# Optimization experiments

Measured on AMD Instinct MI355X. Metric: run time of the kernel, lower is better.

## Reference

```python
import jax, jax.numpy as jnp
import numpy as np

N_NODES = 50000
N_EDGES = 625000
F_IN = 128
F_OUT = 128


def setup_inputs() -> dict:
    key = jax.random.key(0)
    k_x, k_w, k_v, k_r, k_c = jax.random.split(key, 5)
    # Xavier-uniform bound for weight init (matches nn.init.xavier_uniform_)
    bound = float(np.sqrt(6.0 / (F_IN + F_OUT)))
    return {
        "x": jax.random.normal(k_x, (N_NODES, F_IN), dtype=jnp.float32),
        "weight": jax.random.uniform(k_w, (F_IN, F_OUT), minval=-bound, maxval=bound, dtype=jnp.float32),
        "bias": jnp.zeros((F_OUT,), dtype=jnp.float32),
        "edge_vals": jax.random.uniform(k_v, (N_EDGES,), dtype=jnp.float32),
        "edge_rows": jax.random.randint(k_r, (N_EDGES,), 0, N_NODES, dtype=jnp.int32),
        "edge_cols": jax.random.randint(k_c, (N_EDGES,), 0, N_NODES, dtype=jnp.int32),
    }


def reference(x, weight, bias, edge_vals, edge_rows, edge_cols):
    # support = input @ weight  (dense GEMM)  -> [N, F_out]
    support = x @ weight
    # output = spmm(adj, support): for each edge (r, c, v): out[r] += v * support[c]
    msgs = support[edge_cols] * edge_vals[:, None]          # [E, F_out] gather
    out = jax.ops.segment_sum(msgs, edge_rows, num_segments=N_NODES)  # scatter-add
    return out + bias
```

## Files before the change

### kernel.cpp

```cpp
#include <hip/hip_runtime.h>
#include <hip/hip_bf16.h>


#define F_DIM 128

#define NBC 98
#define SLABC 7360
#define NROW_PAD (NBC * 512)

#define BIN_T 256
#define BIN_EPT 16
#define BIN_CHUNK (BIN_T * BIN_EPT)

#define SPLIT_T 512
#define SPLIT_EPT 15

typedef short bf16x8 __attribute__((ext_vector_type(8)));
typedef float f32x4 __attribute__((ext_vector_type(4)));

__device__ __forceinline__ unsigned short f2bf(float f) {
    unsigned int u = __float_as_uint(f);
    u += 0x7FFFu + ((u >> 16) & 1u);
    return (unsigned short)(u >> 16);
}

__global__ void __launch_bounds__(BIN_T)
k1_kernel(const int* __restrict__ rows, const int* __restrict__ cols,
          const float* __restrict__ vals, int* __restrict__ lenC,
          uint2* __restrict__ ebinC, int n_edges,
          const float* __restrict__ w, unsigned short* __restrict__ wt,
          int nbin) {
    __shared__ int lcnt[NBC];
    __shared__ int lbase[NBC];
    __shared__ int garr[NBC];
    __shared__ int partial[128];
    __shared__ uint2 srec[BIN_CHUNK];
    __shared__ unsigned char sbkt[BIN_CHUNK];

    const int t = threadIdx.x;

    if ((int)blockIdx.x >= nbin) {
        int idx = (blockIdx.x - nbin) * BIN_T + t;
        int n = idx >> 7, k = idx & 127;
        wt[n * F_DIM + k] = f2bf(w[k * F_DIM + n]);
        return;
    }

    const int base = blockIdx.x * BIN_CHUNK;

    for (int i = t; i < NBC; i += BIN_T) lcnt[i] = 0;
    __syncthreads();

    unsigned int mykey[BIN_EPT];
    float myval[BIN_EPT];
    bool myok[BIN_EPT];
#pragma unroll
    for (int j = 0; j < BIN_EPT; j++) {
        int e = base + j * BIN_T + t;
        myok[j] = (e < n_edges);
        if (myok[j]) {
            int r = rows[e];
            int c = cols[e];
            myval[j] = vals[e];
            mykey[j] = ((unsigned)r << 16) | (unsigned)c;
            atomicAdd(&lcnt[r >> 9], 1);
        }
    }
    __syncthreads();

    if (t < 128) partial[t] = (t < NBC) ? lcnt[t] : 0;
    __syncthreads();
    for (int d = 1; d < 128; d <<= 1) {
        int u = (t < 128 && t >= d) ? partial[t - d] : 0;
        __syncthreads();
        if (t < 128) partial[t] += u;
        __syncthreads();
    }
    if (t < NBC) {
        lbase[t] = partial[t] - lcnt[t];
        if (lcnt[t] > 0)
            garr[t] = t * SLABC + atomicAdd(&lenC[t], lcnt[t]);
    }
    __syncthreads();
    if (t < NBC) lcnt[t] = lbase[t];
    __syncthreads();

#pragma unroll
    for (int j = 0; j < BIN_EPT; j++) {
        if (myok[j]) {
            int b = (int)(mykey[j] >> 25);
            int p = atomicAdd(&lcnt[b], 1);
            srec[p] = make_uint2(mykey[j], __float_as_uint(myval[j]));
            sbkt[p] = (unsigned char)b;
        }
    }
    __syncthreads();

    const int m = min(BIN_CHUNK, n_edges - base);
    for (int i = t; i < m; i += BIN_T) {
        int b = sbkt[i];
        int dst = garr[b] + (i - lbase[b]);
        if (dst < (b + 1) * SLABC) ebinC[dst] = srec[i];
    }
}

__global__ void __launch_bounds__(SPLIT_T)
split_kernel(const int* __restrict__ lenC, const uint2* __restrict__ ebinC,
             uint2* __restrict__ ebin2, int* __restrict__ roff,
             int* __restrict__ rlen) {
    __shared__ int cnt[SPLIT_T];
    __shared__ int lb[SPLIT_T];
    __shared__ int pos[SPLIT_T];
    __shared__ uint2 srec[SLABC];

    const int b = blockIdx.x;
    const int t = threadIdx.x;
    const int n = min(lenC[b], SLABC);
    const uint2* src = ebinC + (size_t)b * SLABC;

    cnt[t] = 0;
    __syncthreads();

    uint2 myr[SPLIT_EPT];
    int myrow[SPLIT_EPT];
#pragma unroll
    for (int j = 0; j < SPLIT_EPT; j++) {
        int idx = j * SPLIT_T + t;
        myrow[j] = -1;
        if (idx < n) {
            myr[j] = src[idx];
            myrow[j] = (int)((myr[j].x >> 16) & 511u);
            atomicAdd(&cnt[myrow[j]], 1);
        }
    }
    __syncthreads();

    int myc = cnt[t];
    pos[t] = myc;
    __syncthreads();
    for (int d = 1; d < SPLIT_T; d <<= 1) {
        int u = (t >= d) ? pos[t - d] : 0;
        __syncthreads();
        pos[t] += u;
        __syncthreads();
    }
    lb[t] = pos[t] - myc;
    __syncthreads();
    pos[t] = lb[t];
    __syncthreads();

#pragma unroll
    for (int j = 0; j < SPLIT_EPT; j++) {
        if (myrow[j] >= 0) {
            int p = atomicAdd(&pos[myrow[j]], 1);
            srec[p] = myr[j];
        }
    }
    __syncthreads();

    const int gbase = b * SLABC;
    for (int i = t; i < n; i += SPLIT_T)
        ebin2[gbase + i] = srec[i];
    roff[(b << 9) + t] = gbase + lb[t];
    rlen[(b << 9) + t] = myc;
}

__global__ void __launch_bounds__(256)
gemm_mfma_kernel(const float* __restrict__ x, const unsigned short* __restrict__ wt,
                 unsigned short* __restrict__ support) {
    const int tid = threadIdx.x;
    const int wid = tid >> 6;
    const int lane = tid & 63;
    const int l15 = lane & 15;
    const int lhi = lane >> 4;

    const int m0 = blockIdx.x * 16;
    const int n0 = wid * 32;

    const float* xrow = x + (size_t)(m0 + l15) * F_DIM + lhi * 8;
    const unsigned short* wrow0 = wt + (size_t)(n0 + l15) * F_DIM + lhi * 8;
    const unsigned short* wrow1 = wrow0 + 16 * F_DIM;

    f32x4 acc0 = {0.f, 0.f, 0.f, 0.f};
    f32x4 acc1 = {0.f, 0.f, 0.f, 0.f};
#pragma unroll
    for (int k0 = 0; k0 < F_DIM; k0 += 32) {
        float4 xa = *reinterpret_cast<const float4*>(xrow + k0);
        float4 xb = *reinterpret_cast<const float4*>(xrow + k0 + 4);
        bf16x8 a, b0, b1;
        a[0] = (short)f2bf(xa.x); a[1] = (short)f2bf(xa.y);
        a[2] = (short)f2bf(xa.z); a[3] = (short)f2bf(xa.w);
        a[4] = (short)f2bf(xb.x); a[5] = (short)f2bf(xb.y);
        a[6] = (short)f2bf(xb.z); a[7] = (short)f2bf(xb.w);
        b0 = *reinterpret_cast<const bf16x8*>(wrow0 + k0);
        b1 = *reinterpret_cast<const bf16x8*>(wrow1 + k0);
        acc0 = __builtin_amdgcn_mfma_f32_16x16x32_bf16(a, b0, acc0, 0, 0, 0);
        acc1 = __builtin_amdgcn_mfma_f32_16x16x32_bf16(a, b1, acc1, 0, 0, 0);
    }

    unsigned short* sp = support + (size_t)(m0 + 4 * lhi) * F_DIM + n0 + l15;
#pragma unroll
    for (int i = 0; i < 4; i++) {
        sp[(size_t)i * F_DIM]      = f2bf(acc0[i]);
        sp[(size_t)i * F_DIM + 16] = f2bf(acc1[i]);
    }
}

__global__ void __launch_bounds__(256)
bspmm_kernel(const unsigned short* __restrict__ support,
             const uint2* __restrict__ ebin2, const int* __restrict__ roff,
             const int* __restrict__ rlen, const float* __restrict__ bias,
             float* __restrict__ out, int n_nodes) {
    const int row = blockIdx.x * 4 + (threadIdx.x >> 6);
    const int lane = threadIdx.x & 63;
    const unsigned foff = lane * 2u;
    if (row >= n_nodes) return;

    const int s = roff[row];
    const int n = rlen[row];

    float accx = 0.f, accy = 0.f;

#define GATHER(K) (*reinterpret_cast<const unsigned*>(                        \
        support + (size_t)((K) & 0xffffu) * F_DIM + foff))
#define ACC(KEY, VAL, SV)                                                     \
    {                                                                         \
        float v = __uint_as_float(VAL);                                       \
        accx += v * __uint_as_float((SV) << 16);                              \
        accy += v * __uint_as_float((SV) & 0xFFFF0000u);                      \
    }

    int i = 0;
#pragma unroll 1
    for (; i + 3 < n; i += 4) {
        uint2 r0 = ebin2[s + i];
        uint2 r1 = ebin2[s + i + 1];
        uint2 r2 = ebin2[s + i + 2];
        uint2 r3 = ebin2[s + i + 3];
        unsigned s0 = GATHER(r0.x);
        unsigned s1 = GATHER(r1.x);
        unsigned s2 = GATHER(r2.x);
        unsigned s3 = GATHER(r3.x);
        ACC(r0.x, r0.y, s0)
        ACC(r1.x, r1.y, s1)
        ACC(r2.x, r2.y, s2)
        ACC(r3.x, r3.y, s3)
    }
#pragma unroll 1
    for (; i < n; i++) {
        uint2 r = ebin2[s + i];
        unsigned sv = GATHER(r.x);
        ACC(r.x, r.y, sv)
    }
#undef GATHER
#undef ACC

    const float2 bb = *reinterpret_cast<const float2*>(bias + foff);
    float2 o = make_float2(accx + bb.x, accy + bb.y);
    *reinterpret_cast<float2*>(out + (size_t)row * F_DIM + foff) = o;
}

extern "C" void kernel_launch(void* const* d_in, const int* in_sizes, int n_in,
                              void* d_out, int out_size, void* d_ws, size_t ws_size,
                              hipStream_t stream) {
    const float* x      = (const float*)d_in[0];
    const float* weight = (const float*)d_in[1];
    const float* bias   = (const float*)d_in[2];
    const float* evals  = (const float*)d_in[3];
    const int*   erows  = (const int*)d_in[4];
    const int*   ecols  = (const int*)d_in[5];
    float* out = (float*)d_out;

    const int n_nodes = in_sizes[0] / F_DIM;
    const int n_edges = in_sizes[3];

    unsigned short* support = (unsigned short*)d_ws;
    unsigned short* wt      = support + (size_t)n_nodes * F_DIM;
    int* lenC = (int*)(wt + F_DIM * F_DIM);
    int* roff = lenC + 128;
    int* rlen = roff + NROW_PAD;
    uintptr_t ep = (uintptr_t)(rlen + NROW_PAD);
    ep = (ep + 15) & ~(uintptr_t)15;
    uint2* ebinC = (uint2*)ep;
    uint2* ebin2 = ebinC + (size_t)NBC * SLABC;

    hipMemsetAsync(lenC, 0, NBC * sizeof(int), stream);

    int nbin = (n_edges + BIN_CHUNK - 1) / BIN_CHUNK;
    k1_kernel<<<nbin + 64, BIN_T, 0, stream>>>(erows, ecols, evals, lenC,
                                               ebinC, n_edges, weight, wt, nbin);

    split_kernel<<<NBC, SPLIT_T, 0, stream>>>(lenC, ebinC, ebin2, roff, rlen);

    gemm_mfma_kernel<<<n_nodes / 16, 256, 0, stream>>>(x, wt, support);

    bspmm_kernel<<<(n_nodes + 3) / 4, 256, 0, stream>>>(support, ebin2, roff,
                                                        rlen, bias, out, n_nodes);
}
```

Baseline: 93.98 us.

## Use wave-shuffle scans in binning kernels and half-wave edge split in SpMM

The binning and split kernels replace their shared-memory Hillis-Steele prefix scans, which need a barrier per step, with wavefront shuffle scans plus a small cross-wave combine. The binning chunk per block is halved, which launches more blocks and increases contention on the global atomics into lenC. The SpMM kernel now has each half-wave process alternate edges with 8-byte gathers covering 4 features per lane. The two halves are combined with a shuffle-xor at the end, doubling the edges in flight per row at the cost of an extra reduction and idle lanes on the final store.

Result: faster. 90.03 us (-4.2%).

```diff
diff --git a/kernel.cpp b/kernel.cpp
--- a/kernel.cpp
+++ b/kernel.cpp
@@ -9,7 +9,7 @@
 #define NROW_PAD (NBC * 512)
 
 #define BIN_T 256
-#define BIN_EPT 16
+#define BIN_EPT 8
 #define BIN_CHUNK (BIN_T * BIN_EPT)
 
 #define SPLIT_T 512
@@ -33,7 +33,7 @@
     __shared__ int lcnt[NBC];
     __shared__ int lbase[NBC];
     __shared__ int garr[NBC];
-    __shared__ int partial[128];
+    __shared__ int w0sum;
     __shared__ uint2 srec[BIN_CHUNK];
     __shared__ unsigned char sbkt[BIN_CHUNK];
 
@@ -48,7 +48,7 @@
 
     const int base = blockIdx.x * BIN_CHUNK;
 
-    for (int i = t; i < NBC; i += BIN_T) lcnt[i] = 0;
+    if (t < NBC) lcnt[t] = 0;
     __syncthreads();
 
     unsigned int mykey[BIN_EPT];
@@ -68,21 +68,26 @@
     }
     __syncthreads();
 
-    if (t < 128) partial[t] = (t < NBC) ? lcnt[t] : 0;
-    __syncthreads();
-    for (int d = 1; d < 128; d <<= 1) {
-        int u = (t < 128 && t >= d) ? partial[t - d] : 0;
-        __syncthreads();
-        if (t < 128) partial[t] += u;
-        __syncthreads();
-    }
+    const int lane = t & 63;
+    int cval = 0, inc = 0;
+    if (t < 128) {
+        cval = (t < NBC) ? lcnt[t] : 0;
+        inc = cval;
+#pragma unroll
+        for (int d = 1; d < 64; d <<= 1) {
+            int u = __shfl_up(inc, d);
+            if (lane >= d) inc += u;
+        }
+        if (t == 63) w0sum = inc;
+    }
+    __syncthreads();
+    if (t >= 64 && t < 128) inc += w0sum;
     if (t < NBC) {
-        lbase[t] = partial[t] - lcnt[t];
-        if (lcnt[t] > 0)
-            garr[t] = t * SLABC + atomicAdd(&lenC[t], lcnt[t]);
-    }
-    __syncthreads();
-    if (t < NBC) lcnt[t] = lbase[t];
+        int lb = inc - cval;
+        lbase[t] = lb;
+        if (cval > 0) garr[t] = t * SLABC + atomicAdd(&lenC[t], cval);
+        lcnt[t] = lb;
+    }
     __syncthreads();
 
 #pragma unroll
@@ -111,6 +116,7 @@
     __shared__ int cnt[SPLIT_T];
     __shared__ int lb[SPLIT_T];
     __shared__ int pos[SPLIT_T];
+    __shared__ int wsum[8], wbase[8];
     __shared__ uint2 srec[SLABC];
 
     const int b = blockIdx.x;
@@ -135,18 +141,26 @@
     }
     __syncthreads();
 
-    int myc = cnt[t];
-    pos[t] = myc;
-    __syncthreads();
-    for (int d = 1; d < SPLIT_T; d <<= 1) {
-        int u = (t >= d) ? pos[t - d] : 0;
-        __syncthreads();
-        pos[t] += u;
-        __syncthreads();
-    }
-    lb[t] = pos[t] - myc;
-    __syncthreads();
-    pos[t] = lb[t];
+    const int lane = t & 63;
+    const int wv = t >> 6;
+    const int myc = cnt[t];
+    int inc = myc;
+#pragma unroll
+    for (int d = 1; d < 64; d <<= 1) {
+        int u = __shfl_up(inc, d);
+        if (lane >= d) inc += u;
+    }
+    if (lane == 63) wsum[wv] = inc;
+    __syncthreads();
+    if (t == 0) {
+        int run = 0;
+#pragma unroll
+        for (int k = 0; k < 8; k++) { wbase[k] = run; run += wsum[k]; }
+    }
+    __syncthreads();
+    const int excl = wbase[wv] + inc - myc;
+    lb[t] = excl;
+    pos[t] = excl;
     __syncthreads();
 
 #pragma unroll
@@ -213,51 +227,65 @@
              float* __restrict__ out, int n_nodes) {
     const int row = blockIdx.x * 4 + (threadIdx.x >> 6);
     const int lane = threadIdx.x & 63;
-    const unsigned foff = lane * 2u;
+    const int half = lane >> 5;
+    const int l32 = lane & 31;
+    const unsigned coff = l32 * 4u;
     if (row >= n_nodes) return;
 
     const int s = roff[row];
     const int n = rlen[row];
 
-    float accx = 0.f, accy = 0.f;
-
-#define GATHER(K) (*reinterpret_cast<const unsigned*>(                        \
-        support + (size_t)((K) & 0xffffu) * F_DIM + foff))
-#define ACC(KEY, VAL, SV)                                                     \
+    float a0 = 0.f, a1 = 0.f, a2 = 0.f, a3 = 0.f;
+
+#define GATH(K) (*reinterpret_cast<const uint2*>(                             \
+        support + (size_t)((K) & 0xffffu) * F_DIM + coff))
+#define ACC4(VAL, SV)                                                         \
     {                                                                         \
         float v = __uint_as_float(VAL);                                       \
-        accx += v * __uint_as_float((SV) << 16);                              \
-        accy += v * __uint_as_float((SV) & 0xFFFF0000u);                      \
+        a0 += v * __uint_as_float((SV).x << 16);                              \
+        a1 += v * __uint_as_float((SV).x & 0xFFFF0000u);                      \
+        a2 += v * __uint_as_float((SV).y << 16);                              \
+        a3 += v * __uint_as_float((SV).y & 0xFFFF0000u);                      \
     }
 
     int i = 0;
 #pragma unroll 1
-    for (; i + 3 < n; i += 4) {
-        uint2 r0 = ebin2[s + i];
-        uint2 r1 = ebin2[s + i + 1];
-        uint2 r2 = ebin2[s + i + 2];
-        uint2 r3 = ebin2[s + i + 3];
-        unsigned s0 = GATHER(r0.x);
-        unsigned s1 = GATHER(r1.x);
-        unsigned s2 = GATHER(r2.x);
-        unsigned s3 = GATHER(r3.x);
-        ACC(r0.x, r0.y, s0)
-        ACC(r1.x, r1.y, s1)
-        ACC(r2.x, r2.y, s2)
-        ACC(r3.x, r3.y, s3)
+    for (; i + 7 < n; i += 8) {
+        const int j = s + i + half;
+        uint2 r0 = ebin2[j];
+        uint2 r1 = ebin2[j + 2];
+        uint2 r2 = ebin2[j + 4];
+        uint2 r3 = ebin2[j + 6];
+        uint2 s0 = GATH(r0.x);
+        uint2 s1 = GATH(r1.x);
+        uint2 s2 = GATH(r2.x);
+        uint2 s3 = GATH(r3.x);
+        ACC4(r0.y, s0) ACC4(r1.y, s1) ACC4(r2.y, s2) ACC4(r3.y, s3)
     }
 #pragma unroll 1
-    for (; i < n; i++) {
+    for (; i + 1 < n; i += 2) {
+        uint2 r = ebin2[s + i + half];
+        uint2 sv = GATH(r.x);
+        ACC4(r.y, sv)
+    }
+    if (i < n && half == 0) {
         uint2 r = ebin2[s + i];
-        unsigned sv = GATHER(r.x);
-        ACC(r.x, r.y, sv)
-    }
-#undef GATHER
-#undef ACC
-
-    const float2 bb = *reinterpret_cast<const float2*>(bias + foff);
-    float2 o = make_float2(accx + bb.x, accy + bb.y);
-    *reinterpret_cast<float2*>(out + (size_t)row * F_DIM + foff) = o;
+        uint2 sv = GATH(r.x);
+        ACC4(r.y, sv)
+    }
+#undef GATH
+#undef ACC4
+
+    a0 += __shfl_xor(a0, 32);
+    a1 += __shfl_xor(a1, 32);
+    a2 += __shfl_xor(a2, 32);
+    a3 += __shfl_xor(a3, 32);
+
+    if (half == 0) {
+        const float4 bb = *reinterpret_cast<const float4*>(bias + coff);
+        float4 o = make_float4(a0 + bb.x, a1 + bb.y, a2 + bb.z, a3 + bb.w);
+        *reinterpret_cast<float4*>(out + (size_t)row * F_DIM + coff) = o;
+    }
 }
 
 extern "C" void kernel_launch(void* const* d_in, const int* in_sizes, int n_in,
```
